# Kernel tuning notes

Measured on AMD Instinct MI355X. Metric: run time of the kernel, lower is better.

Reference implementation:

```python
import jax, jax.numpy as jnp
import numpy as np

N_NODE, N_EDGE = 8192, 4096
D_NODE, D_EDGE, D_GLOBAL = 64, 16, 8


def _dense(key, fan_in, fan_out):
    kw, kb = jax.random.split(key)
    W = jax.random.normal(kw, (fan_in, fan_out), dtype=jnp.float32) * 0.02
    b = jnp.zeros((fan_out,), dtype=jnp.float32)
    return W, b


def setup_inputs() -> dict:
    key = jax.random.key(0)
    ks = jax.random.split(key, 16)
    nodes = jax.random.normal(ks[0], (N_NODE, D_NODE), dtype=jnp.float32)
    edges = jax.random.normal(ks[1], (N_EDGE, D_EDGE), dtype=jnp.float32)
    globals_ = jax.random.normal(ks[2], (1, D_GLOBAL), dtype=jnp.float32)
    senders = jax.random.randint(ks[3], (N_EDGE,), 0, N_NODE, dtype=jnp.int32)
    receivers = jax.random.randint(ks[4], (N_EDGE,), 0, N_NODE, dtype=jnp.int32)
    # edge MLP: input = concat(edges, nodes[s], nodes[r], globals); widths [N_EDGE]*2
    e_in = D_EDGE + 2 * D_NODE + D_GLOBAL
    eW1, eb1 = _dense(ks[5], e_in, N_EDGE)
    eW2, eb2 = _dense(ks[6], N_EDGE, N_EDGE)
    # node MLP: input = concat(nodes, sent_agg, recv_agg, globals); widths [D_NODE]*2
    n_in = D_NODE + 2 * N_EDGE + D_GLOBAL
    nW1, nb1 = _dense(ks[7], n_in, D_NODE)
    nW2, nb2 = _dense(ks[8], D_NODE, D_NODE)
    return {"nodes": nodes, "edges": edges, "globals_": globals_,
            "senders": senders, "receivers": receivers,
            "eW1": eW1, "eb1": eb1, "eW2": eW2, "eb2": eb2,
            "nW1": nW1, "nb1": nb1, "nW2": nW2, "nb2": nb2}


def reference(nodes, edges, globals_, senders, receivers,
              eW1, eb1, eW2, eb2, nW1, nb1, nW2, nb2):
    n_node, n_edge = nodes.shape[0], edges.shape[0]
    g = globals_[0]  # single graph: broadcast its global feature row
    # --- edge update: concat(edges, sent node feats, received node feats, globals) ---
    g_e = jnp.broadcast_to(g, (n_edge, g.shape[0]))
    e_in = jnp.concatenate([edges, nodes[senders], nodes[receivers], g_e], axis=-1)
    h = jax.nn.relu(e_in @ eW1 + eb1)          # [E, E]
    new_edges = jax.nn.relu(h @ eW2 + eb2)     # [E, E]
    # --- aggregate edges to nodes (jraph default: segment_sum by senders and receivers) ---
    sent_agg = jax.ops.segment_sum(new_edges, senders, num_segments=n_node)
    recv_agg = jax.ops.segment_sum(new_edges, receivers, num_segments=n_node)
    # --- node update: concat(nodes, sent_agg, recv_agg, globals) ---
    g_n = jnp.broadcast_to(g, (n_node, g.shape[0]))
    n_in = jnp.concatenate([nodes, sent_agg, recv_agg, g_n], axis=-1)
    h2 = jax.nn.relu(n_in @ nW1 + nb1)         # [N, D_NODE]
    new_nodes = jax.nn.relu(h2 @ nW2 + nb2)    # [N, D_NODE]
    # globals unchanged (update_global_fn=None)
    return new_nodes, new_edges
```

## Files before the change

### kernel.cpp

```cpp
#include <hip/hip_runtime.h>

typedef unsigned short u16;
typedef unsigned int u32;
typedef unsigned long long u64;
typedef __bf16 bf16x8 __attribute__((ext_vector_type(8)));
typedef float f32x4 __attribute__((ext_vector_type(4)));

static __device__ __forceinline__ float bf2f(u16 u) {
  return __uint_as_float(((u32)u) << 16);
}
static __device__ __forceinline__ u16 f2bf(float f) {
  u32 x = __float_as_uint(f);
  return (u16)((x + 0x7fffu + ((x >> 16) & 1u)) >> 16);
}
static __device__ __forceinline__ void gl_lds16(const u16* g, u16* l) {
  __builtin_amdgcn_global_load_lds(
      (const __attribute__((address_space(1))) void*)g,
      (__attribute__((address_space(3))) void*)l, 16, 0, 0);
}
static __device__ __forceinline__ u64 pack4bf(f32x4 v) {
  u64 r = (u64)f2bf(v[0]);
  r |= (u64)f2bf(v[1]) << 16;
  r |= (u64)f2bf(v[2]) << 32;
  r |= (u64)f2bf(v[3]) << 48;
  return r;
}

static __device__ __forceinline__ void transpose_tile(const float* in, u16* out,
                                                      int K, int N, int Kpad,
                                                      int k0, int n0, int tid,
                                                      u16* t ) {
#pragma unroll
  for (int pass = 0; pass < 4; pass++) {
    int ki = pass * 16 + (tid >> 4);
    int nj = (tid & 15) * 4;
    f32x4 v = {0.f, 0.f, 0.f, 0.f};
    if (k0 + ki < K) v = *(const f32x4*)&in[(long)(k0 + ki) * N + n0 + nj];
    *(u64*)&t[ki * 68 + nj] = pack4bf(v);
  }
  __syncthreads();
#pragma unroll
  for (int pass = 0; pass < 4; pass++) {
    int ni = pass * 16 + (tid >> 4);
    int kj = (tid & 15) * 4;
    if (k0 + kj < Kpad) {
      u64 w = (u64)t[(kj + 0) * 68 + ni] | ((u64)t[(kj + 1) * 68 + ni] << 16) |
              ((u64)t[(kj + 2) * 68 + ni] << 32) | ((u64)t[(kj + 3) * 68 + ni] << 48);
      *(u64*)&out[(long)(n0 + ni) * Kpad + k0 + kj] = w;
    }
  }
}

__global__ __launch_bounds__(256) void k_prep(const float* __restrict__ eW1,
                                              u16* __restrict__ eW1T,
                                              const float* __restrict__ eW2,
                                              u16* __restrict__ eW2T,
                                              const float* __restrict__ edges,
                                              const float* __restrict__ nodes,
                                              const float* __restrict__ g,
                                              const int* __restrict__ senders,
                                              const int* __restrict__ receivers,
                                              u16* __restrict__ ein) {
  __shared__ u16 t[64 * 68];
  const int b = blockIdx.x;
  const int tid = threadIdx.x;
  if (b < 192) {
    transpose_tile(eW1, eW1T, 152, 4096, 160, (b % 3) * 64, (b / 3) * 64, tid, t);
    return;
  }
  if (b < 4288) {
    int bb = b - 192;
    transpose_tile(eW2, eW2T, 4096, 4096, 4096, (bb & 63) * 64, (bb >> 6) * 64, tid, t);
    return;
  }
  int idx = (b - 4288) * 256 + tid;
  int e = idx / 160, x = idx - e * 160;
  float v;
  if (x < 16) v = edges[(long)e * 16 + x];
  else if (x < 80) v = nodes[(long)senders[e] * 64 + (x - 16)];
  else if (x < 144) v = nodes[(long)receivers[e] * 64 + (x - 80)];
  else if (x < 152) v = g[x - 144];
  else v = 0.f;
  ein[idx] = f2bf(v);
}

__global__ __launch_bounds__(256) void k_mid(const float* __restrict__ nW1,
                                             u16* __restrict__ nWmT,
                                             float* __restrict__ accb) {
  __shared__ u16 t[64 * 68];
  const int b = blockIdx.x;
  const int tid = threadIdx.x;
  if (b < 64) {
    transpose_tile(nW1 + 64 * 64, nWmT, 4096, 64, 4096, b * 64, 0, tid, t);
  } else if (b < 128) {
    transpose_tile(nW1 + 4160 * 64, nWmT + (long)64 * 4096, 4096, 64, 4096,
                   (b - 64) * 64, 0, tid, t);
  } else {
    f32x4* a4 = (f32x4*)accb;
    long base = ((long)(b - 128) * 256 + tid) * 8;
#pragma unroll
    for (int j = 0; j < 8; j++) a4[base + j] = {0.f, 0.f, 0.f, 0.f};
  }
}

template <int MODE>
__global__ __launch_bounds__(512, 1) void k_gemm256(const u16* __restrict__ A,
                                                    const u16* __restrict__ BT,
                                                    const float* __restrict__ bias,
                                                    void* __restrict__ C, int N, int K) {
  __shared__ alignas(16) u16 lds[65536];
  const int tid = threadIdx.x;
  const int lane = tid & 63, wid = tid >> 6;
  const int wr = wid >> 2, wc = wid & 3;
  const int orig = blockIdx.x;
  const int xc = orig & 7, jj = orig >> 3;
  const int m0 = (2 * xc + (jj >> 4)) * 256;
  const int n0 = (jj & 15) * 256;
  const int lr = lane & 15, lk = lane >> 4;
  const int swz = (lk ^ ((lr >> 1) & 3)) << 3;
  const int NT = K >> 5;

  const int srow = wid * 16 + (lane >> 2);
  const int sq = ((lane & 3) ^ ((lane >> 3) & 3)) << 3;
  const int sdst = wid * 512 + lane * 8;

  f32x4 acc[8][4];
#pragma unroll
  for (int i = 0; i < 8; i++)
#pragma unroll
    for (int j = 0; j < 4; j++) acc[i][j] = {0.f, 0.f, 0.f, 0.f};

#define STAGE_TILE(T)                                                              \
  {                                                                                \
    const int kt_ = (T) * 32;                                                      \
    u16* Ab_ = &lds[((T) & 3) * 16384];                                            \
    u16* Bb_ = Ab_ + 8192;                                                         \
    gl_lds16(&A[(long)(m0 + srow) * K + kt_ + sq], Ab_ + sdst);                    \
    gl_lds16(&A[(long)(m0 + 128 + srow) * K + kt_ + sq], Ab_ + 4096 + sdst);       \
    gl_lds16(&BT[(long)(n0 + srow) * K + kt_ + sq], Bb_ + sdst);                   \
    gl_lds16(&BT[(long)(n0 + 128 + srow) * K + kt_ + sq], Bb_ + 4096 + sdst);      \
  }

  STAGE_TILE(0)
  STAGE_TILE(1)
  STAGE_TILE(2)

  for (int t = 0; t < NT; t++) {
    if (t < NT - 2) {
      asm volatile("s_waitcnt vmcnt(8)" ::: "memory");
    } else if (t == NT - 2) {
      asm volatile("s_waitcnt vmcnt(4)" ::: "memory");
    } else {
      asm volatile("s_waitcnt vmcnt(0)" ::: "memory");
    }
    __builtin_amdgcn_s_barrier();
    if (t + 3 < NT) STAGE_TILE(t + 3)

    const u16* Ab = &lds[(t & 3) * 16384];
    const u16* Bb = Ab + 8192;
    bf16x8 af[8], bfr[4];
#pragma unroll
    for (int mi = 0; mi < 8; mi++)
      af[mi] = *(const bf16x8*)&Ab[(wr * 128 + mi * 16 + lr) * 32 + swz];
#pragma unroll
    for (int ni = 0; ni < 4; ni++)
      bfr[ni] = *(const bf16x8*)&Bb[(wc * 64 + ni * 16 + lr) * 32 + swz];
#pragma unroll
    for (int mi = 0; mi < 8; mi++)
#pragma unroll
      for (int ni = 0; ni < 4; ni++)
        acc[mi][ni] =
            __builtin_amdgcn_mfma_f32_16x16x32_bf16(af[mi], bfr[ni], acc[mi][ni], 0, 0, 0);
  }
#undef STAGE_TILE

#pragma unroll
  for (int ni = 0; ni < 4; ni++) {
    int col = n0 + wc * 64 + ni * 16 + lr;
    float bb = bias[col];
#pragma unroll
    for (int mi = 0; mi < 8; mi++) {
      int row = m0 + wr * 128 + mi * 16 + lk * 4;
#pragma unroll
      for (int r = 0; r < 4; r++) {
        float v = fmaxf(acc[mi][ni][r] + bb, 0.f);
        if (MODE == 0) ((u16*)C)[(long)(row + r) * N + col] = f2bf(v);
        else ((float*)C)[(long)(row + r) * N + col] = v;
      }
    }
  }
}

__global__ __launch_bounds__(256) void k_scatter_m(const float* __restrict__ E,
                                                   const u16* __restrict__ BT,
                                                   const int* __restrict__ senders,
                                                   const int* __restrict__ receivers,
                                                   float* __restrict__ accb) {
  const int K = 4096;
  __shared__ alignas(16) u16 As[64 * 32];
  __shared__ alignas(16) u16 Bs[128 * 32];
  const int tid = threadIdx.x;
  const int lane = tid & 63, wc = tid >> 6;
  const int m0 = blockIdx.x * 64;
  const int kbase = blockIdx.y * 512;
  const int lr = lane & 15, lk = lane >> 4;
  const int swz = (lk ^ ((lr >> 1) & 3)) << 3;
  const int srow = tid >> 2;
  const int skk = ((tid & 3) ^ ((tid >> 3) & 3)) << 3;

  f32x4 acc[4][2];
#pragma unroll
  for (int i = 0; i < 4; i++)
#pragma unroll
    for (int j = 0; j < 2; j++) acc[i][j] = {0.f, 0.f, 0.f, 0.f};

  for (int kt = kbase; kt < kbase + 512; kt += 32) {
#pragma unroll
    for (int p = 0; p < 2; p++) {
      int idx = p * 256 + tid;
      int r = idx >> 3;
      int kq = idx & 7;
      f32x4 v = *(const f32x4*)&E[(long)(m0 + r) * 4096 + kt + kq * 4];
      int gq = (kq >> 1) ^ ((r >> 1) & 3);
      *(u64*)&As[r * 32 + gq * 8 + (kq & 1) * 4] = pack4bf(v);
    }
#pragma unroll
    for (int rep = 0; rep < 2; rep++) {
      int row = rep * 64 + srow;
      gl_lds16(&BT[(long)row * K + kt + skk], &Bs[rep * 2048 + tid * 8]);
    }
    __syncthreads();
    bf16x8 af[4], bfr[2];
#pragma unroll
    for (int mi = 0; mi < 4; mi++)
      af[mi] = *(const bf16x8*)&As[(mi * 16 + lr) * 32 + swz];
#pragma unroll
    for (int ni = 0; ni < 2; ni++)
      bfr[ni] = *(const bf16x8*)&Bs[(wc * 32 + ni * 16 + lr) * 32 + swz];
#pragma unroll
    for (int mi = 0; mi < 4; mi++)
#pragma unroll
      for (int ni = 0; ni < 2; ni++)
        acc[mi][ni] =
            __builtin_amdgcn_mfma_f32_16x16x32_bf16(af[mi], bfr[ni], acc[mi][ni], 0, 0, 0);
    __syncthreads();
  }
#pragma unroll
  for (int mi = 0; mi < 4; mi++) {
#pragma unroll
    for (int r = 0; r < 4; r++) {
      int e = m0 + mi * 16 + lk * 4 + r;
#pragma unroll
      for (int ni = 0; ni < 2; ni++) {
        int col = wc * 32 + ni * 16 + lr;
        int tgt = (col < 64) ? senders[e] : receivers[e];
        atomicAdd(&accb[(long)tgt * 64 + (col & 63)], acc[mi][ni][r]);
      }
    }
  }
}

__global__ __launch_bounds__(256) void k_final(const float* __restrict__ nodes,
                                               const float* __restrict__ g,
                                               const float* __restrict__ nW1,
                                               const float* __restrict__ nb1,
                                               const float* __restrict__ nW2,
                                               const float* __restrict__ nb2,
                                               const float* __restrict__ zpre,
                                               float* __restrict__ out0) {
  __shared__ float w1[64 * 64];
  __shared__ float w2[64 * 64];
  __shared__ float ns[32 * 64];
  __shared__ float h2[32 * 64];
  __shared__ float gb[64];
  const int tid = threadIdx.x;
  const long n0 = (long)blockIdx.x * 32;
#pragma unroll
  for (int rep = 0; rep < 16; rep++) {
    int idx = rep * 256 + tid;
    w1[idx] = nW1[idx];
    w2[idx] = nW2[idx];
  }
#pragma unroll
  for (int rep = 0; rep < 8; rep++) {
    int idx = rep * 256 + tid;
    ns[idx] = nodes[n0 * 64 + idx];
  }
  if (tid < 64) {
    float s = nb1[tid];
#pragma unroll
    for (int j = 0; j < 8; j++) s += g[j] * nW1[(long)(8256 + j) * 64 + tid];
    gb[tid] = s;
  }
  __syncthreads();
#pragma unroll 2
  for (int rep = 0; rep < 8; rep++) {
    int idx = rep * 256 + tid;
    int i = idx >> 6, c = idx & 63;
    float z = gb[c] + zpre[(n0 + i) * 64 + c];
#pragma unroll 8
    for (int k = 0; k < 64; k++) z += ns[i * 64 + k] * w1[k * 64 + c];
    h2[idx] = fmaxf(z, 0.f);
  }
  __syncthreads();
#pragma unroll 2
  for (int rep = 0; rep < 8; rep++) {
    int idx = rep * 256 + tid;
    int i = idx >> 6, c = idx & 63;
    float z = nb2[c];
#pragma unroll 8
    for (int k = 0; k < 64; k++) z += h2[i * 64 + k] * w2[k * 64 + c];
    out0[(n0 + i) * 64 + c] = fmaxf(z, 0.f);
  }
}

extern "C" void kernel_launch(void* const* d_in, const int* in_sizes, int n_in,
                              void* d_out, int out_size, void* d_ws, size_t ws_size,
                              hipStream_t stream) {
  const float* nodes = (const float*)d_in[0];
  const float* edges = (const float*)d_in[1];
  const float* g = (const float*)d_in[2];
  const int* senders = (const int*)d_in[3];
  const int* receivers = (const int*)d_in[4];
  const float* eW1 = (const float*)d_in[5];
  const float* eb1 = (const float*)d_in[6];
  const float* eW2 = (const float*)d_in[7];
  const float* eb2 = (const float*)d_in[8];
  const float* nW1 = (const float*)d_in[9];
  const float* nb1 = (const float*)d_in[10];
  const float* nW2 = (const float*)d_in[11];
  const float* nb2 = (const float*)d_in[12];

  char* ws = (char*)d_ws;
  u16* eW1T = (u16*)(ws + 0);
  float* accb = (float*)(ws + 0);
  u16* ein = (u16*)(ws + 2097152);
  u16* nWmT = (u16*)(ws + 2097152);
  u16* eW2T = (u16*)(ws + 3407872);
  u16* h = (u16*)(ws + 36962304);

  float* out_nodes = (float*)d_out;
  float* out_edges = (float*)d_out + 524288;

  dim3 b256(256);
  k_prep<<<6848, b256, 0, stream>>>(eW1, eW1T, eW2, eW2T, edges, nodes, g,
                                    senders, receivers, ein);
  k_gemm256<0><<<dim3(256), dim3(512), 0, stream>>>(ein, eW1T, eb1, h, 4096, 160);
  k_mid<<<192, b256, 0, stream>>>(nW1, nWmT, accb);
  k_gemm256<1><<<dim3(256), dim3(512), 0, stream>>>(h, eW2T, eb2, out_edges, 4096, 4096);
  k_scatter_m<<<dim3(64, 8), b256, 0, stream>>>(out_edges, nWmT, senders, receivers, accb);
  k_final<<<256, b256, 0, stream>>>(nodes, g, nW1, nb1, nW2, nb2, accb, out_nodes);
}
```

Measured before the change: 212.8 us.

## Shrink GEMM tiles to 128x256 with 4 waves, 2 blocks per CU, triple buffering

The GEMM kernel is retiled from 256x256 blocks of 8 waves to 128x256 blocks of 4 waves, launching 512 blocks with two resident per CU. The LDS ring drops from four stages to three, using about 72KB per block instead of 128KB. The aim is better occupancy and latency hiding across co-resident blocks, and more blocks to fill the CUs. In exchange each block reuses its B tile over fewer rows, which raises global traffic per FLOP, and the pipeline is shallower.

```diff
diff --git a/kernel.cpp b/kernel.cpp
--- a/kernel.cpp
+++ b/kernel.cpp
@@ -104,25 +104,28 @@
 }
 
 template <int MODE>
-__global__ __launch_bounds__(512, 1) void k_gemm256(const u16* __restrict__ A,
+__global__ __launch_bounds__(256, 2) void k_gemm128(const u16* __restrict__ A,
                                                     const u16* __restrict__ BT,
                                                     const float* __restrict__ bias,
                                                     void* __restrict__ C, int N, int K) {
-  __shared__ alignas(16) u16 lds[65536];
-  const int tid = threadIdx.x;
-  const int lane = tid & 63, wid = tid >> 6;
-  const int wr = wid >> 2, wc = wid & 3;
+  __shared__ alignas(16) u16 lds[36864];
+  const int tid = threadIdx.x;
+  const int lane = tid & 63, wc = tid >> 6;
   const int orig = blockIdx.x;
   const int xc = orig & 7, jj = orig >> 3;
-  const int m0 = (2 * xc + (jj >> 4)) * 256;
+  const int m0 = (4 * xc + (jj >> 4)) * 128;
   const int n0 = (jj & 15) * 256;
   const int lr = lane & 15, lk = lane >> 4;
   const int swz = (lk ^ ((lr >> 1) & 3)) << 3;
   const int NT = K >> 5;
 
-  const int srow = wid * 16 + (lane >> 2);
-  const int sq = ((lane & 3) ^ ((lane >> 3) & 3)) << 3;
-  const int sdst = wid * 512 + lane * 8;
+  const int sq = ((tid & 3) ^ ((tid >> 3) & 3)) << 3;
+  const long a_r0 = (long)(m0 + (tid >> 2)) * K + sq;
+  const long a_r1 = a_r0 + (long)64 * K;
+  const long b_r0 = (long)(n0 + (tid >> 2)) * K + sq;
+  const long b_r1 = b_r0 + (long)64 * K;
+  const long b_r2 = b_r0 + (long)128 * K;
+  const long b_r3 = b_r0 + (long)192 * K;
 
   f32x4 acc[8][4];
 #pragma unroll
@@ -130,38 +133,40 @@
 #pragma unroll
     for (int j = 0; j < 4; j++) acc[i][j] = {0.f, 0.f, 0.f, 0.f};
 
-#define STAGE_TILE(T)                                                              \
-  {                                                                                \
-    const int kt_ = (T) * 32;                                                      \
-    u16* Ab_ = &lds[((T) & 3) * 16384];                                            \
-    u16* Bb_ = Ab_ + 8192;                                                         \
-    gl_lds16(&A[(long)(m0 + srow) * K + kt_ + sq], Ab_ + sdst);                    \
-    gl_lds16(&A[(long)(m0 + 128 + srow) * K + kt_ + sq], Ab_ + 4096 + sdst);       \
-    gl_lds16(&BT[(long)(n0 + srow) * K + kt_ + sq], Bb_ + sdst);                   \
-    gl_lds16(&BT[(long)(n0 + 128 + srow) * K + kt_ + sq], Bb_ + 4096 + sdst);      \
-  }
-
-  STAGE_TILE(0)
-  STAGE_TILE(1)
-  STAGE_TILE(2)
-
+#define STAGE_TILE(T, BUF)                          \
+  {                                                 \
+    const int kt_ = (T) * 32;                       \
+    u16* Ab_ = &lds[(BUF) * 12288];                 \
+    u16* Bb_ = Ab_ + 4096;                          \
+    gl_lds16(&A[a_r0 + kt_], Ab_ + tid * 8);        \
+    gl_lds16(&A[a_r1 + kt_], Ab_ + 2048 + tid * 8); \
+    gl_lds16(&BT[b_r0 + kt_], Bb_ + tid * 8);       \
+    gl_lds16(&BT[b_r1 + kt_], Bb_ + 2048 + tid * 8);\
+    gl_lds16(&BT[b_r2 + kt_], Bb_ + 4096 + tid * 8);\
+    gl_lds16(&BT[b_r3 + kt_], Bb_ + 6144 + tid * 8);\
+  }
+
+  STAGE_TILE(0, 0)
+  STAGE_TILE(1, 1)
+
+  int b0 = 0;
   for (int t = 0; t < NT; t++) {
-    if (t < NT - 2) {
-      asm volatile("s_waitcnt vmcnt(8)" ::: "memory");
-    } else if (t == NT - 2) {
-      asm volatile("s_waitcnt vmcnt(4)" ::: "memory");
+    if (t < NT - 1) {
+      asm volatile("s_waitcnt vmcnt(6)" ::: "memory");
     } else {
       asm volatile("s_waitcnt vmcnt(0)" ::: "memory");
     }
     __builtin_amdgcn_s_barrier();
-    if (t + 3 < NT) STAGE_TILE(t + 3)
-
-    const u16* Ab = &lds[(t & 3) * 16384];
-    const u16* Bb = Ab + 8192;
+    if (t + 2 < NT) {
+      int sb = b0 ? b0 - 1 : 2;
+      STAGE_TILE(t + 2, sb)
+    }
+    const u16* Ab = &lds[b0 * 12288];
+    const u16* Bb = Ab + 4096;
     bf16x8 af[8], bfr[4];
 #pragma unroll
     for (int mi = 0; mi < 8; mi++)
-      af[mi] = *(const bf16x8*)&Ab[(wr * 128 + mi * 16 + lr) * 32 + swz];
+      af[mi] = *(const bf16x8*)&Ab[(mi * 16 + lr) * 32 + swz];
 #pragma unroll
     for (int ni = 0; ni < 4; ni++)
       bfr[ni] = *(const bf16x8*)&Bb[(wc * 64 + ni * 16 + lr) * 32 + swz];
@@ -171,6 +176,7 @@
       for (int ni = 0; ni < 4; ni++)
         acc[mi][ni] =
             __builtin_amdgcn_mfma_f32_16x16x32_bf16(af[mi], bfr[ni], acc[mi][ni], 0, 0, 0);
+    b0 = (b0 == 2) ? 0 : b0 + 1;
   }
 #undef STAGE_TILE
 
@@ -180,7 +186,7 @@
     float bb = bias[col];
 #pragma unroll
     for (int mi = 0; mi < 8; mi++) {
-      int row = m0 + wr * 128 + mi * 16 + lk * 4;
+      int row = m0 + mi * 16 + lk * 4;
 #pragma unroll
       for (int r = 0; r < 4; r++) {
         float v = fmaxf(acc[mi][ni][r] + bb, 0.f);
@@ -345,9 +351,9 @@
   dim3 b256(256);
   k_prep<<<6848, b256, 0, stream>>>(eW1, eW1T, eW2, eW2T, edges, nodes, g,
                                     senders, receivers, ein);
-  k_gemm256<0><<<dim3(256), dim3(512), 0, stream>>>(ein, eW1T, eb1, h, 4096, 160);
+  k_gemm128<0><<<dim3(512), b256, 0, stream>>>(ein, eW1T, eb1, h, 4096, 160);
   k_mid<<<192, b256, 0, stream>>>(nW1, nWmT, accb);
-  k_gemm256<1><<<dim3(256), dim3(512), 0, stream>>>(h, eW2T, eb2, out_edges, 4096, 4096);
+  k_gemm128<1><<<dim3(512), b256, 0, stream>>>(h, eW2T, eb2, out_edges, 4096, 4096);
   k_scatter_m<<<dim3(64, 8), b256, 0, stream>>>(out_edges, nWmT, senders, receivers, accb);
   k_final<<<256, b256, 0, stream>>>(nodes, g, nW1, nb1, nW2, nb2, accb, out_nodes);
 }
```

Result: slower. 225.9 us (+6.1%).
